# Kernel optimization log

Measured on AMD Instinct MI355X. Metric: run time of the kernel, lower is better.

The kernel has to match this reference:

```python
import jax, jax.numpy as jnp
import numpy as np

NUM_ENTRIES = 8192
CODE_DIM = 256
COMMITMENT_COST = 0.25


def setup_inputs() -> dict:
    key = jax.random.key(0)
    k_z, k_cb = jax.random.split(key)
    z = jax.random.normal(k_z, (32, 1024, CODE_DIM), dtype=jnp.float32)
    # nn.Embedding weight init: uniform(-1/num_entries, 1/num_entries)
    bound = 1.0 / NUM_ENTRIES
    codebook = jax.random.uniform(k_cb, (NUM_ENTRIES, CODE_DIM), dtype=jnp.float32,
                                  minval=-bound, maxval=bound)
    return {"z": z, "codebook": codebook}


def reference(z, codebook):
    z_flat = z.reshape(-1, CODE_DIM)  # [N, D]
    # squared euclidean distances: ||z||^2 + ||e||^2 - 2 z.e^T  -> [N, K]
    distances = (jnp.sum(z_flat ** 2, axis=1, keepdims=True)
                 + jnp.sum(codebook ** 2, axis=1)
                 - 2.0 * jnp.matmul(z_flat, codebook.T))
    indices = jnp.argmin(distances, axis=1)  # [N]
    z_q = codebook[indices]  # [N, D]
    codebook_loss = jnp.mean((z_q - jax.lax.stop_gradient(z_flat)) ** 2)
    commitment_loss = jnp.mean((jax.lax.stop_gradient(z_q) - z_flat) ** 2)
    loss = codebook_loss + COMMITMENT_COST * commitment_loss
    # straight-through estimator
    z_q_st = z_flat + jax.lax.stop_gradient(z_q - z_flat)
    z_q_st = z_q_st.reshape(z.shape)
    return z_q_st, loss, indices.reshape(z.shape[:-1])
```

## Files before the change

kernel.cpp:

```cpp
#include <hip/hip_runtime.h>

typedef unsigned int u32;
typedef unsigned long long u64;
typedef unsigned short ushort_t;

#define NROWS 32768
#define KENT  8192
#define DDIM  256
#define ND_TOTAL 8388608
#define CAP   1048576u
#define LBUF  2048

#define WS_COUNTER   0
#define WS_A         64
#define WS_MARG      131136
#define WS_ROWTHR    262208
#define WS_KEYS      393280
#define WS_CANDS     655424
#define WS_ZH        9044032
#define WS_EH        25821248
#define WS_LOSS      30015552
#define WS_NEEDED    30019648ull

typedef __attribute__((ext_vector_type(8))) short s16x8;
typedef __attribute__((ext_vector_type(4))) float f32x4;

__device__ __forceinline__ unsigned short bf16_rne(float f) {
  u32 u = __float_as_uint(f);
  u32 r = (u + 0x7fffu + ((u >> 16) & 1u)) >> 16;
  return (unsigned short)r;
}

__device__ __forceinline__ u32 fkey(float s) {
  u32 b = __float_as_uint(s);
  u32 mask = (u32)((int)b >> 31);
  return b ^ (mask | 0x80000000u);
}
__device__ __forceinline__ float unkey(u32 k) {
  u32 b = (k & 0x80000000u) ? (k ^ 0x80000000u) : ~k;
  return __uint_as_float(b);
}
#define KEY_INF 0xFF800000u

__device__ __forceinline__ void gll16(const void* g, void* l) {
  __builtin_amdgcn_global_load_lds((const __attribute__((address_space(1))) void*)g,
                                   (__attribute__((address_space(3))) void*)l, 16, 0, 0);
}

__global__ __launch_bounds__(256) void vq_prep_z(
    const float* __restrict__ z, unsigned short* __restrict__ zh,
    float* __restrict__ A, float* __restrict__ marg, u64* __restrict__ keys) {
  const int wid = threadIdx.x >> 6, lane = threadIdx.x & 63;
  const int row = blockIdx.x * 4 + wid;
  float4 v = ((const float4*)z)[(size_t)row * 64 + lane];
  ushort4 h;
  h.x = bf16_rne(v.x); h.y = bf16_rne(v.y); h.z = bf16_rne(v.z); h.w = bf16_rne(v.w);
  *(ushort4*)&zh[(size_t)row * 256 + lane * 4] = h;
  double s  = (double)v.x * v.x + (double)v.y * v.y + (double)v.z * v.z + (double)v.w * v.w;
  double s1 = fabs((double)v.x) + fabs((double)v.y) + fabs((double)v.z) + fabs((double)v.w);
#pragma unroll
  for (int m = 1; m <= 32; m <<= 1) { s += __shfl_xor(s, m, 64); s1 += __shfl_xor(s1, m, 64); }
  if (lane == 0) {
    float Af = (float)s;
    u32 bits = __float_as_uint(Af);
    float ulpA = __uint_as_float((bits & 0x7f800000u) - (23u << 23));
    A[row] = Af;
    marg[row] = 4.0f * ulpA + 3.86e-6f * (float)s1 + 4e-6f;
    keys[row] = ~0ull;
  }
}

__global__ __launch_bounds__(256) void vq_prep_e(
    const float* __restrict__ cb, unsigned short* __restrict__ eh,
    u32* __restrict__ counter) {
  if (blockIdx.x == 0 && threadIdx.x == 0) *counter = 0u;
  const int wid = threadIdx.x >> 6, lane = threadIdx.x & 63;
  const int row = blockIdx.x * 4 + wid;
  float4 v = ((const float4*)cb)[(size_t)row * 64 + wid * 0 + lane];
  ushort4 h;
  h.x = bf16_rne(v.x); h.y = bf16_rne(v.y); h.z = bf16_rne(v.z); h.w = bf16_rne(v.w);
  *(ushort4*)&eh[(size_t)row * 256 + lane * 4] = h;
}

__global__ __launch_bounds__(512, 2) void vq_fused8(
    const ushort_t* __restrict__ zh, const ushort_t* __restrict__ eh,
    const float* __restrict__ z, const float* __restrict__ cb,
    const float* __restrict__ Ag, const float* __restrict__ marg,
    float* __restrict__ rowthr, u64* __restrict__ keys,
    u64* __restrict__ cands, u32* __restrict__ counter) {
  __shared__ __align__(16) ushort_t Bsm[2][32768];
  __shared__ u32 rowKey[128];
  __shared__ u64 lbuf[LBUF];
  __shared__ u32 lcount;
  __shared__ float thrF[128];

  const int tid = threadIdx.x, w = tid >> 6, lane = tid & 63;
  const int l15 = lane & 15, l4 = lane >> 4;
  const int wrow = (w >> 2) * 64, wcol = (w & 3) * 64;
  const int rowbase = blockIdx.x * 128;

  if (tid < 128) rowKey[tid] = KEY_INF;
  if (tid == 0) lcount = 0u;

  s16x8 areg[4][8];
#pragma unroll
  for (int fi = 0; fi < 4; ++fi)
#pragma unroll
    for (int kt = 0; kt < 8; ++kt)
      areg[fi][kt] = *(const s16x8*)(zh + (size_t)(rowbase + wrow + fi * 16 + l15) * 256
                                        + kt * 32 + l4 * 8);
  float mg[4][4];
#pragma unroll
  for (int fi = 0; fi < 4; ++fi)
#pragma unroll
    for (int rg = 0; rg < 4; ++rg)
      mg[fi][rg] = marg[rowbase + wrow + fi * 16 + l4 * 4 + rg];

  const int t0 = w * 128 + lane, t1 = t0 + 64;
  const int e0 = t0 >> 2, e1 = t1 >> 2;
  const ushort_t* gs0 = eh + (size_t)e0 * 256 + (((t0 & 3) ^ ((e0 >> 1) & 3)) * 8);
  const ushort_t* gs1 = eh + (size_t)e1 * 256 + (((t1 & 3) ^ ((e1 >> 1) & 3)) * 8);

#define ISSUE_STAGE(BUF, CT, S) do {                                              \
    _Pragma("unroll")                                                             \
    for (int kk_ = 0; kk_ < 4; ++kk_) {                                           \
      size_t o_ = (size_t)(CT) * 65536 + (size_t)((S) * 4 + kk_) * 32;            \
      gll16(gs0 + o_, &Bsm[(BUF)][kk_ * 8192 + w * 1024]);                        \
      gll16(gs1 + o_, &Bsm[(BUF)][kk_ * 8192 + w * 1024 + 512]);                  \
    }                                                                             \
  } while (0)

  int boff[4];
#pragma unroll
  for (int fj = 0; fj < 4; ++fj) {
    int e = wcol + fj * 16 + l15;
    boff[fj] = e * 32 + (l4 ^ ((e >> 1) & 3)) * 8;
  }

  f32x4 acc[4][4];

#define COMPUTE_STAGE(S) do {                                                     \
    __builtin_amdgcn_s_setprio(1);                                                \
    _Pragma("unroll")                                                             \
    for (int kk_ = 0; kk_ < 4; ++kk_) {                                           \
      s16x8 bv[4];                                                                \
      _Pragma("unroll")                                                           \
      for (int fj = 0; fj < 4; ++fj)                                              \
        bv[fj] = *(const s16x8*)&Bsm[(S)][kk_ * 8192 + boff[fj]];                 \
      _Pragma("unroll")                                                           \
      for (int fi = 0; fi < 4; ++fi)                                              \
        _Pragma("unroll")                                                         \
        for (int fj = 0; fj < 4; ++fj)                                            \
          acc[fi][fj] = __builtin_amdgcn_mfma_f32_16x16x32_bf16(                  \
              areg[fi][(S) * 4 + kk_], bv[fj], acc[fi][fj], 0, 0, 0);             \
    }                                                                             \
    __builtin_amdgcn_s_setprio(0);                                                \
  } while (0)

  ISSUE_STAGE(0, 0, 0);
  __syncthreads();

#pragma unroll 1
  for (int it = 0; it <= 32; ++it) {
    const int ct = (it < 32) ? it : 0;
#pragma unroll
    for (int fi = 0; fi < 4; ++fi)
#pragma unroll
      for (int fj = 0; fj < 4; ++fj) acc[fi][fj] = (f32x4){0.f, 0.f, 0.f, 0.f};

    ISSUE_STAGE(1, ct, 1);
    COMPUTE_STAGE(0);
    __syncthreads();

    if (it < 32) {
      const int ctn = (it + 1 < 32) ? (it + 1) : 0;
      ISSUE_STAGE(0, ctn, 0);
    }
    COMPUTE_STAGE(1);

#pragma unroll
    for (int fi = 0; fi < 4; ++fi) {
#pragma unroll
      for (int rg = 0; rg < 4; ++rg) {
        const int rl = wrow + fi * 16 + l4 * 4 + rg;
        float amax = acc[fi][0][rg];
#pragma unroll
        for (int fj = 1; fj < 4; ++fj) amax = fmaxf(amax, acc[fi][fj][rg]);
        float smin = -2.0f * amax;
        u32 kc = rowKey[rl];
        u32 nk = fkey(smin);
        if (nk < kc) atomicMin(&rowKey[rl], nk);
        if (it >= 1) {
          const float thr = unkey(kc) + mg[fi][rg];
          const float hthr = -0.5f * thr;
          const int nb = ct * 256 + wcol + l15;
#pragma unroll
          for (int fj = 0; fj < 4; ++fj) {
            if (acc[fi][fj][rg] >= hthr) {
              float sv = -2.0f * acc[fi][fj][rg];
              u64 pk = ((u64)__float_as_uint(sv) << 32) | ((u64)(u32)rl << 13)
                     | (u64)(u32)(nb + fj * 16);
              u32 lp = atomicAdd(&lcount, 1u);
              if (lp < LBUF) lbuf[lp] = pk;
              else {
                u32 p = atomicAdd(counter, 1u);
                if (p < CAP) cands[p] = pk + ((u64)(u32)rowbase << 13);
              }
            }
          }
        }
      }
    }
    __syncthreads();
  }

  if (tid < 128) {
    float t = unkey(rowKey[tid]) + marg[rowbase + tid];
    thrF[tid] = t;
    rowthr[rowbase + tid] = t;
  }
  __syncthreads();
  u32 tl = lcount; if (tl > LBUF) tl = LBUF;
  for (u32 i = tid; i < tl; i += 512) {
    u64 c = lbuf[i];
    float s = __uint_as_float((u32)(c >> 32));
    const int rl = (int)((c >> 13) & 127u);
    const int n  = (int)(c & 0x1fffu);
    if (s > thrF[rl]) continue;
    const int m = rowbase + rl;
    const float4* zr = (const float4*)(z + (size_t)m * 256);
    const float4* er = (const float4*)(cb + (size_t)n * 256);
    float acc1 = 0.f;
    for (int j = 0; j < 64; ++j) {
      float4 a = zr[j], b = er[j];
      acc1 = fmaf(a.x, b.x, acc1); acc1 = fmaf(a.y, b.y, acc1);
      acc1 = fmaf(a.z, b.z, acc1); acc1 = fmaf(a.w, b.w, acc1);
    }
    float d = fmaf(-2.f, acc1, Ag[m]);
    u64 key = ((u64)__float_as_uint(d) << 32) | (u64)(u32)n;
    atomicMin(&keys[m], key);
  }
#undef ISSUE_STAGE
#undef COMPUTE_STAGE
}

__global__ __launch_bounds__(256) void vq_exact2(
    const float* __restrict__ z, const float* __restrict__ cb,
    const float* __restrict__ A, const float* __restrict__ rowthr,
    const u64* __restrict__ cands, const u32* __restrict__ counter,
    u64* __restrict__ keys) {
  u32 cnt = *counter; if (cnt > CAP) cnt = CAP;
  for (u32 i = blockIdx.x * 256 + threadIdx.x; i < cnt; i += gridDim.x * 256) {
    u64 c = cands[i];
    float s = __uint_as_float((u32)(c >> 32));
    const int m = (int)((c >> 13) & 0x7fffu);
    const int n = (int)(c & 0x1fffu);
    if (s > rowthr[m]) continue;
    const float4* zr = (const float4*)(z + (size_t)m * 256);
    const float4* er = (const float4*)(cb + (size_t)n * 256);
    float acc = 0.f;
    for (int j = 0; j < 64; ++j) {
      float4 a = zr[j], b = er[j];
      acc = fmaf(a.x, b.x, acc); acc = fmaf(a.y, b.y, acc);
      acc = fmaf(a.z, b.z, acc); acc = fmaf(a.w, b.w, acc);
    }
    float d = fmaf(-2.f, acc, A[m]);
    u64 key = ((u64)__float_as_uint(d) << 32) | (u64)(u32)n;
    atomicMin(&keys[m], key);
  }
}

__global__ __launch_bounds__(256) void vq_gather_new(
    const float* __restrict__ z, const float* __restrict__ cb,
    const u64* __restrict__ keys, float* __restrict__ idx_out,
    float* __restrict__ zq_out, double* __restrict__ loss_part) {
  __shared__ double lred[4];
  const int tid = threadIdx.x;
  const int rl = tid >> 2, part = tid & 3;
  const int R = blockIdx.x * 64 + rl;
  const int bi = (int)(keys[R] & 0x1fffull);
  if (part == 0) idx_out[R] = (float)bi;
  const float4* zr = (const float4*)z + (size_t)R * 64 + part * 16;
  const float4* er = (const float4*)cb + (size_t)bi * 64 + part * 16;
  float4* orow = (float4*)zq_out + (size_t)R * 64 + part * 16;
  double lsum = 0.0;
#pragma unroll
  for (int i = 0; i < 16; ++i) {
    float4 zv = zr[i], ev = er[i];
    float dx = ev.x - zv.x, dy = ev.y - zv.y, dz = ev.z - zv.z, dw = ev.w - zv.w;
    float4 o; o.x = zv.x + dx; o.y = zv.y + dy; o.z = zv.z + dz; o.w = zv.w + dw;
    orow[i] = o;
    lsum += (double)dx * dx + (double)dy * dy + (double)dz * dz + (double)dw * dw;
  }
#pragma unroll
  for (int o = 32; o > 0; o >>= 1) lsum += __shfl_down(lsum, o, 64);
  if ((tid & 63) == 0) lred[tid >> 6] = lsum;
  __syncthreads();
  if (tid == 0) loss_part[blockIdx.x] = lred[0] + lred[1] + lred[2] + lred[3];
}

__global__ void vq_finalize_kernel(const double* __restrict__ loss_part,
                                   float* __restrict__ loss_out) {
  if (threadIdx.x == 0 && blockIdx.x == 0) {
    double s = 0.0;
    for (int b = 0; b < 512; ++b) s += loss_part[b];
    *loss_out = (float)(s / (double)ND_TOTAL * 1.25);
  }
}

__global__ __launch_bounds__(256) void vq_argmin_fb(
    const float* __restrict__ z, const float* __restrict__ cb,
    float* __restrict__ idx_out) {
  __shared__ float4 zs[64 * 64];
  const int tid = threadIdx.x;
  const int tc = tid & 15, tr = tid >> 4;
  const int rowbase = blockIdx.x * 64;
  const float4* zg4 = (const float4*)z;
  const float4* cb4 = (const float4*)cb;
  const int swz = (tr & 3) << 1;
#pragma unroll
  for (int i = 0; i < 16; ++i) {
    int idx = i * 256 + tid;
    int row = idx >> 6, dq = idx & 63;
    int col = dq ^ (((row >> 2) & 3) << 1);
    zs[row * 64 + col] = zg4[(size_t)rowbase * 64 + idx];
  }
  __syncthreads();
  float A[4];
#pragma unroll
  for (int r = 0; r < 4; ++r) {
    int row = tr * 4 + r;
    float p = 0.f;
#pragma unroll
    for (int j = 0; j < 4; ++j) {
      int dq = tc + 16 * j;
      float4 v = zs[row * 64 + (dq ^ swz)];
      p = fmaf(v.x, v.x, p); p = fmaf(v.y, v.y, p);
      p = fmaf(v.z, v.z, p); p = fmaf(v.w, v.w, p);
    }
#pragma unroll
    for (int m = 1; m <= 8; m <<= 1) p += __shfl_xor(p, m, 64);
    A[r] = p;
  }
  float b1[4] = {INFINITY, INFINITY, INFINITY, INFINITY};
  int   i1[4] = {0x7fffffff, 0x7fffffff, 0x7fffffff, 0x7fffffff};
  for (int kt = 0; kt < 64; ++kt) {
    const int e0 = kt * 128 + tc * 8;
    const float4* eb = cb4 + (size_t)e0 * 64;
    float acc[4][8];
#pragma unroll
    for (int r = 0; r < 4; ++r)
#pragma unroll
      for (int c = 0; c < 8; ++c) acc[r][c] = 0.f;
#pragma unroll 2
    for (int dq = 0; dq < 64; ++dq) {
      float4 ev[8];
#pragma unroll
      for (int c = 0; c < 8; ++c) ev[c] = eb[c * 64 + dq];
      const int col = dq ^ swz;
      float4 zv[4];
#pragma unroll
      for (int r = 0; r < 4; ++r) zv[r] = zs[(tr * 4 + r) * 64 + col];
#pragma unroll
      for (int r = 0; r < 4; ++r)
#pragma unroll
        for (int c = 0; c < 8; ++c) {
          acc[r][c] = fmaf(zv[r].x, ev[c].x, acc[r][c]);
          acc[r][c] = fmaf(zv[r].y, ev[c].y, acc[r][c]);
          acc[r][c] = fmaf(zv[r].z, ev[c].z, acc[r][c]);
          acc[r][c] = fmaf(zv[r].w, ev[c].w, acc[r][c]);
        }
    }
#pragma unroll
    for (int c = 0; c < 8; ++c)
#pragma unroll
      for (int r = 0; r < 4; ++r) {
        float d = A[r] - 2.0f * acc[r][c];
        if (d < b1[r]) { b1[r] = d; i1[r] = e0 + c; }
      }
  }
  __syncthreads();
  float* rs = (float*)zs;
  int*   ri = (int*)(rs + 64 * 16);
#pragma unroll
  for (int r = 0; r < 4; ++r) {
    rs[(tr * 4 + r) * 16 + tc] = b1[r];
    ri[(tr * 4 + r) * 16 + tc] = i1[r];
  }
  __syncthreads();
  if (tid < 64) {
    float B = INFINITY; int I = 0x7fffffff;
#pragma unroll
    for (int c = 0; c < 16; ++c) {
      float v = rs[tid * 16 + c];
      int  ix = ri[tid * 16 + c];
      if (v < B || (v == B && ix < I)) { B = v; I = ix; }
    }
    idx_out[rowbase + tid] = (float)I;
  }
}

__global__ __launch_bounds__(256) void vq_gather_fb(
    const float* __restrict__ z, const float* __restrict__ cb,
    const float* __restrict__ idx_out, float* __restrict__ zq_out,
    double* __restrict__ loss_part) {
  __shared__ double lred[4];
  const int tid = threadIdx.x;
  const int rl = tid >> 2, part = tid & 3;
  const int R = blockIdx.x * 64 + rl;
  const int bi = (int)idx_out[R];
  const float4* zr = (const float4*)z + (size_t)R * 64 + part * 16;
  const float4* er = (const float4*)cb + (size_t)bi * 64 + part * 16;
  float4* orow = (float4*)zq_out + (size_t)R * 64 + part * 16;
  double lsum = 0.0;
#pragma unroll
  for (int i = 0; i < 16; ++i) {
    float4 zv = zr[i], ev = er[i];
    float dx = ev.x - zv.x, dy = ev.y - zv.y, dz = ev.z - zv.z, dw = ev.w - zv.w;
    float4 o; o.x = zv.x + dx; o.y = zv.y + dy; o.z = zv.z + dz; o.w = zv.w + dw;
    orow[i] = o;
    lsum += (double)dx * dx + (double)dy * dy + (double)dz * dz + (double)dw * dw;
  }
#pragma unroll
  for (int o = 32; o > 0; o >>= 1) lsum += __shfl_down(lsum, o, 64);
  if ((tid & 63) == 0) lred[tid >> 6] = lsum;
  __syncthreads();
  if (tid == 0) loss_part[blockIdx.x] = lred[0] + lred[1] + lred[2] + lred[3];
}

extern "C" void kernel_launch(void* const* d_in, const int* in_sizes, int n_in,
                              void* d_out, int out_size, void* d_ws, size_t ws_size,
                              hipStream_t stream) {
  const float* z  = (const float*)d_in[0];
  const float* cb = (const float*)d_in[1];
  float* out = (float*)d_out;
  float* zq_out   = out;
  float* loss_out = out + ND_TOTAL;
  float* idx_out  = out + ND_TOTAL + 1;

  if (ws_size >= WS_NEEDED) {
    char* ws = (char*)d_ws;
    u32* counter          = (u32*)(ws + WS_COUNTER);
    float* A              = (float*)(ws + WS_A);
    float* marg           = (float*)(ws + WS_MARG);
    float* rowthr         = (float*)(ws + WS_ROWTHR);
    u64* keys             = (u64*)(ws + WS_KEYS);
    u64* cands            = (u64*)(ws + WS_CANDS);
    unsigned short* zh    = (unsigned short*)(ws + WS_ZH);
    unsigned short* eh    = (unsigned short*)(ws + WS_EH);
    double* loss_part     = (double*)(ws + WS_LOSS);

    vq_prep_z<<<NROWS / 4, 256, 0, stream>>>(z, zh, A, marg, keys);
    vq_prep_e<<<KENT / 4, 256, 0, stream>>>(cb, eh, counter);
    vq_fused8<<<NROWS / 128, 512, 0, stream>>>(zh, eh, z, cb, A, marg, rowthr, keys, cands, counter);
    vq_exact2<<<256, 256, 0, stream>>>(z, cb, A, rowthr, cands, counter, keys);
    vq_gather_new<<<NROWS / 64, 256, 0, stream>>>(z, cb, keys, idx_out, zq_out, loss_part);
    vq_finalize_kernel<<<1, 64, 0, stream>>>(loss_part, loss_out);
  } else {
    double* loss_part = (double*)d_ws;
    vq_argmin_fb<<<NROWS / 64, 256, 0, stream>>>(z, cb, idx_out);
    vq_gather_fb<<<NROWS / 64, 256, 0, stream>>>(z, cb, idx_out, zq_out, loss_part);
    vq_finalize_kernel<<<1, 64, 0, stream>>>(loss_part, loss_out);
  }
}
```

Before: 369.7 us.

## Stage z tile in LDS and pipeline codebook per 32-wide k-slice

Moves the bf16 z row tile from per-thread registers (areg[4][8]) into LDS, loaded once with async global-to-LDS copies. The codebook double buffer shrinks from 4-kslice stages to single 32-wide k-slices, so the loop now issues the next slice while computing the current one, with a barrier every k-step. The per-row margins move from registers to shared memory. The goal is to free VGPRs and cut LDS footprint; launch bounds change to one block per SM. The cost is eight barriers per codebook tile instead of two, and extra LDS reads for the A fragments.

```diff
diff --git a/kernel.cpp b/kernel.cpp
--- a/kernel.cpp
+++ b/kernel.cpp
@@ -76,20 +76,22 @@
   if (blockIdx.x == 0 && threadIdx.x == 0) *counter = 0u;
   const int wid = threadIdx.x >> 6, lane = threadIdx.x & 63;
   const int row = blockIdx.x * 4 + wid;
-  float4 v = ((const float4*)cb)[(size_t)row * 64 + wid * 0 + lane];
+  float4 v = ((const float4*)cb)[(size_t)row * 64 + lane];
   ushort4 h;
   h.x = bf16_rne(v.x); h.y = bf16_rne(v.y); h.z = bf16_rne(v.z); h.w = bf16_rne(v.w);
   *(ushort4*)&eh[(size_t)row * 256 + lane * 4] = h;
 }
 
-__global__ __launch_bounds__(512, 2) void vq_fused8(
+__global__ __launch_bounds__(512, 1) void vq_fused9(
     const ushort_t* __restrict__ zh, const ushort_t* __restrict__ eh,
     const float* __restrict__ z, const float* __restrict__ cb,
     const float* __restrict__ Ag, const float* __restrict__ marg,
     float* __restrict__ rowthr, u64* __restrict__ keys,
     u64* __restrict__ cands, u32* __restrict__ counter) {
-  __shared__ __align__(16) ushort_t Bsm[2][32768];
+  __shared__ __align__(16) ushort_t Asm[8][4096];
+  __shared__ __align__(16) ushort_t Bsm[2][8192];
   __shared__ u32 rowKey[128];
+  __shared__ float mgS[128];
   __shared__ u64 lbuf[LBUF];
   __shared__ u32 lcount;
   __shared__ float thrF[128];
@@ -99,84 +101,73 @@
   const int wrow = (w >> 2) * 64, wcol = (w & 3) * 64;
   const int rowbase = blockIdx.x * 128;
 
-  if (tid < 128) rowKey[tid] = KEY_INF;
+  if (tid < 128) {
+    rowKey[tid] = KEY_INF;
+    mgS[tid] = marg[rowbase + tid];
+  }
   if (tid == 0) lcount = 0u;
 
-  s16x8 areg[4][8];
-#pragma unroll
-  for (int fi = 0; fi < 4; ++fi)
-#pragma unroll
-    for (int kt = 0; kt < 8; ++kt)
-      areg[fi][kt] = *(const s16x8*)(zh + (size_t)(rowbase + wrow + fi * 16 + l15) * 256
-                                        + kt * 32 + l4 * 8);
-  float mg[4][4];
-#pragma unroll
-  for (int fi = 0; fi < 4; ++fi)
-#pragma unroll
-    for (int rg = 0; rg < 4; ++rg)
-      mg[fi][rg] = marg[rowbase + wrow + fi * 16 + l4 * 4 + rg];
+#pragma unroll
+  for (int i = 0; i < 8; ++i) {
+    const int t = i * 64 + lane;
+    const int e = t >> 2;
+    const int gc = (t & 3) ^ ((e >> 1) & 3);
+    gll16(zh + (size_t)(rowbase + e) * 256 + w * 32 + gc * 8, &Asm[w][i * 512]);
+  }
 
   const int t0 = w * 128 + lane, t1 = t0 + 64;
   const int e0 = t0 >> 2, e1 = t1 >> 2;
   const ushort_t* gs0 = eh + (size_t)e0 * 256 + (((t0 & 3) ^ ((e0 >> 1) & 3)) * 8);
   const ushort_t* gs1 = eh + (size_t)e1 * 256 + (((t1 & 3) ^ ((e1 >> 1) & 3)) * 8);
 
-#define ISSUE_STAGE(BUF, CT, S) do {                                              \
-    _Pragma("unroll")                                                             \
-    for (int kk_ = 0; kk_ < 4; ++kk_) {                                           \
-      size_t o_ = (size_t)(CT) * 65536 + (size_t)((S) * 4 + kk_) * 32;            \
-      gll16(gs0 + o_, &Bsm[(BUF)][kk_ * 8192 + w * 1024]);                        \
-      gll16(gs1 + o_, &Bsm[(BUF)][kk_ * 8192 + w * 1024 + 512]);                  \
-    }                                                                             \
+#define ISSUE(BUF, CT, KT) do {                                        \
+    size_t o_ = (size_t)(CT) * 65536 + (size_t)(KT) * 32;              \
+    gll16(gs0 + o_, &Bsm[(BUF)][w * 1024]);                            \
+    gll16(gs1 + o_, &Bsm[(BUF)][w * 1024 + 512]);                      \
   } while (0)
 
-  int boff[4];
-#pragma unroll
-  for (int fj = 0; fj < 4; ++fj) {
-    int e = wcol + fj * 16 + l15;
-    boff[fj] = e * 32 + (l4 ^ ((e >> 1) & 3)) * 8;
-  }
-
-  f32x4 acc[4][4];
-
-#define COMPUTE_STAGE(S) do {                                                     \
-    __builtin_amdgcn_s_setprio(1);                                                \
-    _Pragma("unroll")                                                             \
-    for (int kk_ = 0; kk_ < 4; ++kk_) {                                           \
-      s16x8 bv[4];                                                                \
-      _Pragma("unroll")                                                           \
-      for (int fj = 0; fj < 4; ++fj)                                              \
-        bv[fj] = *(const s16x8*)&Bsm[(S)][kk_ * 8192 + boff[fj]];                 \
-      _Pragma("unroll")                                                           \
-      for (int fi = 0; fi < 4; ++fi)                                              \
-        _Pragma("unroll")                                                         \
-        for (int fj = 0; fj < 4; ++fj)                                            \
-          acc[fi][fj] = __builtin_amdgcn_mfma_f32_16x16x32_bf16(                  \
-              areg[fi][(S) * 4 + kk_], bv[fj], acc[fi][fj], 0, 0, 0);             \
-    }                                                                             \
-    __builtin_amdgcn_s_setprio(0);                                                \
-  } while (0)
-
-  ISSUE_STAGE(0, 0, 0);
-  __syncthreads();
+  int aoff[4], boff[4];
+#pragma unroll
+  for (int f = 0; f < 4; ++f) {
+    int ea = wrow + f * 16 + l15;
+    aoff[f] = ea * 32 + (l4 ^ ((ea >> 1) & 3)) * 8;
+    int eb = wcol + f * 16 + l15;
+    boff[f] = eb * 32 + (l4 ^ ((eb >> 1) & 3)) * 8;
+  }
+
+  ISSUE(0, 0, 0);
+  __syncthreads();
+  int cur = 0;
 
 #pragma unroll 1
   for (int it = 0; it <= 32; ++it) {
     const int ct = (it < 32) ? it : 0;
+    f32x4 acc[4][4];
 #pragma unroll
     for (int fi = 0; fi < 4; ++fi)
 #pragma unroll
       for (int fj = 0; fj < 4; ++fj) acc[fi][fj] = (f32x4){0.f, 0.f, 0.f, 0.f};
 
-    ISSUE_STAGE(1, ct, 1);
-    COMPUTE_STAGE(0);
-    __syncthreads();
-
-    if (it < 32) {
-      const int ctn = (it + 1 < 32) ? (it + 1) : 0;
-      ISSUE_STAGE(0, ctn, 0);
-    }
-    COMPUTE_STAGE(1);
+#pragma unroll
+    for (int kt = 0; kt < 8; ++kt) {
+      if (kt < 7)       ISSUE(cur ^ 1, ct, kt + 1);
+      else if (it < 32) ISSUE(cur ^ 1, (it + 1 < 32) ? (it + 1) : 0, 0);
+      s16x8 af[4], bv[4];
+#pragma unroll
+      for (int f = 0; f < 4; ++f) {
+        af[f] = *(const s16x8*)&Asm[kt][aoff[f]];
+        bv[f] = *(const s16x8*)&Bsm[cur][boff[f]];
+      }
+      __builtin_amdgcn_s_setprio(1);
+#pragma unroll
+      for (int fi = 0; fi < 4; ++fi)
+#pragma unroll
+        for (int fj = 0; fj < 4; ++fj)
+          acc[fi][fj] = __builtin_amdgcn_mfma_f32_16x16x32_bf16(af[fi], bv[fj], acc[fi][fj], 0, 0, 0);
+      __builtin_amdgcn_s_setprio(0);
+      __syncthreads();
+      cur ^= 1;
+    }
 
 #pragma unroll
     for (int fi = 0; fi < 4; ++fi) {
@@ -191,7 +182,7 @@
         u32 nk = fkey(smin);
         if (nk < kc) atomicMin(&rowKey[rl], nk);
         if (it >= 1) {
-          const float thr = unkey(kc) + mg[fi][rg];
+          const float thr = unkey(kc) + mgS[rl];
           const float hthr = -0.5f * thr;
           const int nb = ct * 256 + wcol + l15;
 #pragma unroll
@@ -211,11 +202,11 @@
         }
       }
     }
-    __syncthreads();
-  }
-
+  }
+
+  __syncthreads();
   if (tid < 128) {
-    float t = unkey(rowKey[tid]) + marg[rowbase + tid];
+    float t = unkey(rowKey[tid]) + mgS[tid];
     thrF[tid] = t;
     rowthr[rowbase + tid] = t;
   }
@@ -240,8 +231,7 @@
     u64 key = ((u64)__float_as_uint(d) << 32) | (u64)(u32)n;
     atomicMin(&keys[m], key);
   }
-#undef ISSUE_STAGE
-#undef COMPUTE_STAGE
+#undef ISSUE
 }
 
 __global__ __launch_bounds__(256) void vq_exact2(
@@ -452,7 +442,7 @@
 
     vq_prep_z<<<NROWS / 4, 256, 0, stream>>>(z, zh, A, marg, keys);
     vq_prep_e<<<KENT / 4, 256, 0, stream>>>(cb, eh, counter);
-    vq_fused8<<<NROWS / 128, 512, 0, stream>>>(zh, eh, z, cb, A, marg, rowthr, keys, cands, counter);
+    vq_fused9<<<NROWS / 128, 512, 0, stream>>>(zh, eh, z, cb, A, marg, rowthr, keys, cands, counter);
     vq_exact2<<<256, 256, 0, stream>>>(z, cb, A, rowthr, cands, counter, keys);
     vq_gather_new<<<NROWS / 64, 256, 0, stream>>>(z, cb, keys, idx_out, zq_out, loss_part);
     vq_finalize_kernel<<<1, 64, 0, stream>>>(loss_part, loss_out);
```

New measurement: 354.0 us. 4.3% less time.
